# Performance work log

Measured on AMD Instinct MI355X. Metric: run time of the kernel, lower is better.

The kernel has to match this reference:

```python
import jax, jax.numpy as jnp
import numpy as np

N = 50000      # n_nodes
E = 800000     # n_edges (before self loops)
DIN = 128      # in_channels
H = 4          # heads
C = 32         # out_channels per head  (H*C == DIN -> residual is Identity)
EPS = 1e-5
NEG_SLOPE = 0.2


def layer_norm(x, g, b):
    m = jnp.mean(x, axis=-1, keepdims=True)
    v = jnp.mean((x - m) ** 2, axis=-1, keepdims=True)
    return (x - m) * jax.lax.rsqrt(v + EPS) * g + b


def setup_inputs() -> dict:
    key = jax.random.key(0)
    ks = jax.random.split(key, 14)
    s = 1.0 / np.sqrt(DIN)
    return {
        "x": jax.random.normal(ks[0], (N, DIN), dtype=jnp.float32),
        "edge_index": jax.random.randint(ks[1], (2, E), 0, N, dtype=jnp.int64),
        "ln1_g": jnp.ones((DIN,), jnp.float32),
        "ln1_b": jnp.zeros((DIN,), jnp.float32),
        "W": jax.random.normal(ks[2], (DIN, H * C), jnp.float32) * s,
        "att_src": jax.random.normal(ks[3], (H, C), jnp.float32) * (1.0 / np.sqrt(C)),
        "att_dst": jax.random.normal(ks[4], (H, C), jnp.float32) * (1.0 / np.sqrt(C)),
        "gat_b": jnp.zeros((H * C,), jnp.float32),
        "ln2_g": jnp.ones((H * C,), jnp.float32),
        "ln2_b": jnp.zeros((H * C,), jnp.float32),
        "w1": jax.random.normal(ks[5], (H * C, 2 * H * C), jnp.float32) * (1.0 / np.sqrt(H * C)),
        "b1": jnp.zeros((2 * H * C,), jnp.float32),
        "w2": jax.random.normal(ks[6], (2 * H * C, H * C), jnp.float32) * (1.0 / np.sqrt(2 * H * C)),
        "b2": jnp.zeros((H * C,), jnp.float32),
    }


def gat_conv(h, src, dst, W, att_src, att_dst, gat_b, n):
    # linear projection per head: (n, H, C)
    xh = (h @ W).reshape(n, H, C)
    # per-node attention logits: (n, H)
    a_src = jnp.einsum("nhc,hc->nh", xh, att_src)
    a_dst = jnp.einsum("nhc,hc->nh", xh, att_dst)
    # edge scores + segment softmax over destination nodes
    alpha = jax.nn.leaky_relu(a_src[src] + a_dst[dst], NEG_SLOPE)  # (e, H)
    amax = jax.ops.segment_max(alpha, dst, num_segments=n)
    alpha = jnp.exp(alpha - amax[dst])
    denom = jax.ops.segment_sum(alpha, dst, num_segments=n)
    alpha = alpha / denom[dst]
    # weighted aggregation of source features
    msg = xh[src] * alpha[:, :, None]                                # (e, H, C)
    out = jax.ops.segment_sum(msg, dst, num_segments=n)              # (n, H, C)
    return out.reshape(n, H * C) + gat_b


def reference(x, edge_index, ln1_g, ln1_b, W, att_src, att_dst, gat_b,
              ln2_g, ln2_b, w1, b1, w2, b2):
    n = x.shape[0]
    # add self loops (PyG GATConv default add_self_loops=True)
    loops = jnp.arange(n, dtype=edge_index.dtype)
    src = jnp.concatenate([edge_index[0], loops])
    dst = jnp.concatenate([edge_index[1], loops])

    h = layer_norm(x, ln1_g, ln1_b)
    h = gat_conv(h, src, dst, W, att_src, att_dst, gat_b, n)
    h = h + x  # residual is Identity since in_channels == heads*out_channels
    hn = layer_norm(h, ln2_g, ln2_b)
    ffn = jax.nn.gelu(hn @ w1 + b1, approximate=False) @ w2 + b2
    return h + ffn
```

## Files before the change

kernel.cpp:

```cpp
#include <hip/hip_runtime.h>

#define DIN 128
#define HEADS 4
#define CPH 32
#define NEG_SLOPE 0.2f
#define LN_EPS 1e-5f
#define NPB 16
#define CS 4096
#define CE 512

typedef short bf16x8 __attribute__((ext_vector_type(8)));
typedef float f32x4 __attribute__((ext_vector_type(4)));
typedef float f32x2 __attribute__((ext_vector_type(2)));

__device__ __forceinline__ float wave_allsum(float v) {
#pragma unroll
    for (int off = 32; off > 0; off >>= 1) v += __shfl_down(v, off, 64);
    return __shfl(v, 0, 64);
}

__device__ __forceinline__ unsigned short f2bf(float f) {
    unsigned int b = __float_as_uint(f);
    b += 0x7FFFu + ((b >> 16) & 1u);
    return (unsigned short)(b >> 16);
}
__device__ __forceinline__ float bf2f(unsigned short u) {
    return __uint_as_float(((unsigned int)u) << 16);
}

#define ABST 136
#define HST  264
#define SRST 132

__global__ __launch_bounds__(256) void k_hist_pack(
    const int* __restrict__ ei, unsigned int* __restrict__ cnt, int E, int Et, int HB,
    const float* __restrict__ w1, const float* __restrict__ w2, const float* __restrict__ W,
    unsigned short* __restrict__ wp1, unsigned short* __restrict__ wp2,
    unsigned short* __restrict__ wpW)
{
    int bid = blockIdx.x;
    if (bid < HB) {
        int base = bid * CS + threadIdx.x;
#pragma unroll
        for (int i = 0; i < CS / 256; ++i) {
            int e = base + i * 256;
            if (e >= Et) break;
            int d = (e < E) ? ei[E + e] : (e - E);
            atomicAdd(&cnt[d], 1u);
        }
    } else {
        int idx = (bid - HB) * 256 + threadIdx.x;
        if (idx < 32768) {
            int j = idx & 7, lane = (idx >> 3) & 63, tk = idx >> 9;
            int ks = tk & 3, tile = tk >> 2;
            int k = ks * 32 + ((lane >> 4) << 3) + j;
            int n = tile * 16 + (lane & 15);
            wp1[idx] = f2bf(w1[k * 256 + n]);
        } else if (idx < 65536) {
            int i2 = idx - 32768;
            int j = i2 & 7, lane = (i2 >> 3) & 63, tk = i2 >> 9;
            int ks = tk & 7, tile = tk >> 3;
            int k = ks * 32 + ((lane >> 4) << 3) + j;
            int n = tile * 16 + (lane & 15);
            wp2[i2] = f2bf(w2[k * 128 + n]);
        } else {
            int i3 = idx - 65536;
            int j = i3 & 7, lane = (i3 >> 3) & 63, tk = i3 >> 9;
            int ks = tk & 3, tile = tk >> 2;
            int k = ks * 32 + ((lane >> 4) << 3) + j;
            int n = tile * 16 + (lane & 15);
            wpW[i3] = f2bf(W[k * 128 + n]);
        }
    }
}

__global__ __launch_bounds__(256) void k_scan_fused(
    const unsigned int* __restrict__ cnt,
    unsigned int* __restrict__ done, unsigned int* __restrict__ flag,
    unsigned int* __restrict__ bsum, unsigned int* __restrict__ boff,
    unsigned int* __restrict__ row, unsigned int* __restrict__ pos, int N, int Et)
{
    __shared__ unsigned int ws[4];
    __shared__ unsigned int s_tot;
    __shared__ int s_last;
    __shared__ unsigned int s_base;
    int t = threadIdx.x;
    int lane = t & 63, wv = t >> 6;
    int bid = blockIdx.x;
    int nb = gridDim.x;
    int i = bid * 256 + t;

    unsigned int v = (i < N) ? cnt[i] : 0u;
    unsigned int s = v;
#pragma unroll
    for (int off = 1; off < 64; off <<= 1) {
        unsigned int a = (unsigned int)__shfl_up((int)s, off, 64);
        if (lane >= off) s += a;
    }
    if (lane == 63) ws[wv] = s;
    __syncthreads();
    if (t == 0) {
        unsigned int a0 = ws[0], a1 = ws[1], a2 = ws[2], a3 = ws[3];
        ws[0] = 0u; ws[1] = a0; ws[2] = a0 + a1; ws[3] = a0 + a1 + a2;
        s_tot = a0 + a1 + a2 + a3;
    }
    __syncthreads();
    unsigned int excl = ws[wv] + (s - v);

    if (t == 0) {
        __hip_atomic_store(&bsum[bid], s_tot, __ATOMIC_RELEASE, __HIP_MEMORY_SCOPE_AGENT);
        unsigned int old = __hip_atomic_fetch_add(done, 1u, __ATOMIC_ACQ_REL, __HIP_MEMORY_SCOPE_AGENT);
        s_last = (old == (unsigned int)(nb - 1)) ? 1 : 0;
    }
    __syncthreads();

    if (s_last) {
        unsigned int bv = (t < nb) ? __hip_atomic_load(&bsum[t], __ATOMIC_ACQUIRE, __HIP_MEMORY_SCOPE_AGENT) : 0u;
        unsigned int sc = bv;
#pragma unroll
        for (int off = 1; off < 64; off <<= 1) {
            unsigned int a = (unsigned int)__shfl_up((int)sc, off, 64);
            if (lane >= off) sc += a;
        }
        if (lane == 63) ws[wv] = sc;
        __syncthreads();
        if (t == 0) {
            unsigned int a0 = ws[0], a1 = ws[1], a2 = ws[2];
            ws[0] = 0u; ws[1] = a0; ws[2] = a0 + a1; ws[3] = a0 + a1 + a2;
        }
        __syncthreads();
        if (t < nb) boff[t] = ws[wv] + (sc - bv);
        __syncthreads();
        if (t == 0) __hip_atomic_store(flag, 1u, __ATOMIC_RELEASE, __HIP_MEMORY_SCOPE_AGENT);
    }

    if (t == 0) {
        while (__hip_atomic_load(flag, __ATOMIC_ACQUIRE, __HIP_MEMORY_SCOPE_AGENT) == 0u)
            __builtin_amdgcn_s_sleep(8);
        s_base = boff[bid];
    }
    __syncthreads();
    unsigned int base = s_base;
    if (i < N) { row[i] = base + excl; pos[i] = base + excl; }
    if (bid == 0 && t == 0) row[N] = (unsigned int)Et;
}

__global__ __launch_bounds__(256) void k_scatter_proj(
    const int* __restrict__ ei, unsigned int* __restrict__ pos,
    int* __restrict__ srcs, int E, int N, int Et, int SB,
    const float* __restrict__ x,
    const float* __restrict__ g1, const float* __restrict__ b1,
    const unsigned short* __restrict__ wpW,
    const float* __restrict__ att_src, const float* __restrict__ att_dst,
    unsigned short* __restrict__ xhb, float* __restrict__ a_src, float* __restrict__ a_dst)
{
    __shared__ __align__(16) unsigned short A_bf[NPB * ABST];
    __shared__ __align__(16) unsigned short sxh[NPB * ABST];
    int bid = blockIdx.x;
    int t = threadIdx.x;

    if (bid < SB) {
        int base = bid * CS + t;
#pragma unroll
        for (int i = 0; i < CS / 256; ++i) {
            int e = base + i * 256;
            if (e >= Et) break;
            int d = (e < E) ? ei[E + e] : (e - E);
            int s = (e < E) ? ei[e] : d;
            unsigned int p = atomicAdd(&pos[d], 1u);
            srcs[p] = s;
        }
        return;
    }

    int w = t >> 6, lane = t & 63;
    int quad = lane >> 4, l15 = lane & 15;
    int nbase = (bid - SB) * NPB;

#pragma unroll
    for (int i = 0; i < 4; ++i) {
        int nn = w * 4 + i;
        int n = nbase + nn;
        float x0 = 0.f, x1 = 0.f;
        if (n < N) { x0 = x[n * DIN + lane]; x1 = x[n * DIN + 64 + lane]; }
        float mean = wave_allsum(x0 + x1) * (1.0f / DIN);
        float d0 = x0 - mean, d1 = x1 - mean;
        float var = wave_allsum(d0 * d0 + d1 * d1) * (1.0f / DIN);
        float rstd = rsqrtf(var + LN_EPS);
        A_bf[nn * ABST + lane]      = f2bf(d0 * rstd * g1[lane]      + b1[lane]);
        A_bf[nn * ABST + 64 + lane] = f2bf(d1 * rstd * g1[64 + lane] + b1[64 + lane]);
    }
    __syncthreads();

    {
        int arow = l15 * ABST;
        bf16x8 afrag[4];
#pragma unroll
        for (int ks = 0; ks < 4; ++ks)
            afrag[ks] = *(const bf16x8*)&A_bf[arow + ks * 32 + quad * 8];
#pragma unroll
        for (int nt = 0; nt < 2; ++nt) {
            int tile = w * 2 + nt;
            f32x4 acc = {0.f, 0.f, 0.f, 0.f};
#pragma unroll
            for (int ks = 0; ks < 4; ++ks) {
                bf16x8 bfrag = *(const bf16x8*)&wpW[(((tile * 4 + ks) * 64 + lane) << 3)];
                acc = __builtin_amdgcn_mfma_f32_16x16x32_bf16(afrag[ks], bfrag, acc, 0, 0, 0);
            }
            int col = tile * 16 + l15;
#pragma unroll
            for (int reg = 0; reg < 4; ++reg)
                sxh[(quad * 4 + reg) * ABST + col] = f2bf(acc[reg]);
        }
    }
    __syncthreads();

    {
        int node = t >> 4, off = (t & 15) * 8;
        int n = nbase + node;
        if (n < N)
            *(uint4*)&xhb[(size_t)n * DIN + off] = *(const uint4*)&sxh[node * ABST + off];
    }

    {
        int node = w * 4 + (lane >> 4);
        int h = (lane >> 2) & 3, sub = lane & 3;
        float s1 = 0.f, s2 = 0.f;
#pragma unroll
        for (int i = 0; i < 8; ++i) {
            int c = h * CPH + sub * 8 + i;
            float v = bf2f(sxh[node * ABST + c]);
            s1 += v * att_src[c];
            s2 += v * att_dst[c];
        }
        s1 += __shfl_down(s1, 1, 64); s2 += __shfl_down(s2, 1, 64);
        s1 += __shfl_down(s1, 2, 64); s2 += __shfl_down(s2, 2, 64);
        int n = nbase + node;
        if (sub == 0 && n < N) {
            a_src[n * HEADS + h] = s1;
            a_dst[n * HEADS + h] = s2;
        }
    }
}

__global__ __launch_bounds__(256, 6) void k_agg_final(
    const unsigned int* __restrict__ row, const int* __restrict__ srcs,
    const float* __restrict__ a_src, const float* __restrict__ a_dst,
    const uint2* __restrict__ xhb2,
    const float* __restrict__ x,
    const float* __restrict__ gat_b,
    const float* __restrict__ g2, const float* __restrict__ b2g,
    const unsigned short* __restrict__ wp1, const float* __restrict__ bb1,
    const unsigned short* __restrict__ wp2, const float* __restrict__ bb2,
    float* __restrict__ out, int N)
{
    __shared__ __align__(16) unsigned char smem[21248];
    float*          shres  = (float*)smem;
    unsigned short* A_bf   = (unsigned short*)(smem + 8448);
    unsigned short* hid_bf = (unsigned short*)(smem + 12800);
    float*          s_p    = (float*)smem;
    int*            s_srcs = (int*)(smem + 8192);
    float*          s_adl  = (float*)(smem + 10240);
    int*            s_rowl = (int*)(smem + 10496);

    int t = threadIdx.x;
    int w = t >> 6, lane = t & 63;
    int quad = lane >> 4, l15 = lane & 15;
    int nbase = blockIdx.x * NPB;
    int half = lane >> 5;
    int li   = lane & 31;
    int h2   = li >> 3;

    f32x2 gbp, g2p, b2p;
    {
        const f32x2* gb2 = (const f32x2*)gat_b;
        const f32x2* gg2 = (const f32x2*)g2;
        const f32x2* bb2v = (const f32x2*)b2g;
        gbp = gb2[lane]; g2p = gg2[lane]; b2p = bb2v[lane];
    }

    if (t <= NPB) {
        int idx = nbase + t; if (idx > N) idx = N;
        s_rowl[t] = (int)row[idx];
    }
    if (t < 64) {
        int d = nbase + (t >> 2);
        s_adl[t] = (d < N) ? a_dst[d * HEADS + (t & 3)] : 0.f;
    }

    int nend = nbase + NPB; if (nend > N) nend = N;
    int estart = (int)row[nbase];
    int eend = (int)row[nend];

    int wr[5];
#pragma unroll
    for (int j = 0; j < 5; ++j) {
        int idx = nbase + w * 4 + j; if (idx > N) idx = N;
        wr[j] = (int)row[idx];
    }

    float o4[4][4];
    float den4[4];
#pragma unroll
    for (int i = 0; i < 4; ++i) {
        den4[i] = 0.f;
#pragma unroll
        for (int c = 0; c < 4; ++c) o4[i][c] = 0.f;
    }

    for (int cbase = estart; cbase < eend; cbase += CE) {
        int cnum = eend - cbase; if (cnum > CE) cnum = CE;
        int cend = cbase + cnum;
        __syncthreads();

        for (int e = t; e < cnum; e += 256) {
            int ge = cbase + e;
            int s = srcs[ge];
            s_srcs[e] = s;
            int node = 0;
#pragma unroll
            for (int k = 1; k <= NPB; ++k) node += (ge >= s_rowl[k]) ? 1 : 0;
            float4 as4 = *(const float4*)&a_src[s * 4];
            float4 ad4 = *(const float4*)&s_adl[node * 4];
            float4 pv;
            float a0 = as4.x + ad4.x; a0 = fmaxf(a0, NEG_SLOPE * a0); pv.x = __expf(a0);
            float a1 = as4.y + ad4.y; a1 = fmaxf(a1, NEG_SLOPE * a1); pv.y = __expf(a1);
            float a2 = as4.z + ad4.z; a2 = fmaxf(a2, NEG_SLOPE * a2); pv.z = __expf(a2);
            float a3 = as4.w + ad4.w; a3 = fmaxf(a3, NEG_SLOPE * a3); pv.w = __expf(a3);
            *(float4*)&s_p[e * 4] = pv;
        }
        __syncthreads();

#pragma unroll
        for (int i = 0; i < 4; ++i) {
            int lo = wr[i] > cbase ? wr[i] : cbase;
            int hi = wr[i + 1] < cend ? wr[i + 1] : cend;
            if (lo >= hi) continue;
            int e = lo - cbase;
            int eh = hi - cbase;
            float p0_ = o4[i][0], p1_ = o4[i][1], p2_ = o4[i][2], p3_ = o4[i][3];
            float den_ = den4[i];
            for (; e + 16 <= eh; e += 16) {
                uint2 uu[8]; float pp[8];
#pragma unroll
                for (int j = 0; j < 8; ++j) {
                    int s = s_srcs[e + 2 * j + half];
                    uu[j] = xhb2[s * 32 + li];
                }
#pragma unroll
                for (int j = 0; j < 8; ++j) pp[j] = s_p[((e + 2 * j + half) << 2) + h2];
#pragma unroll
                for (int j = 0; j < 8; ++j) {
                    den_ += pp[j];
                    p0_ += pp[j] * __uint_as_float(uu[j].x << 16);
                    p1_ += pp[j] * __uint_as_float(uu[j].x & 0xFFFF0000u);
                    p2_ += pp[j] * __uint_as_float(uu[j].y << 16);
                    p3_ += pp[j] * __uint_as_float(uu[j].y & 0xFFFF0000u);
                }
            }
            for (; e + 8 <= eh; e += 8) {
                uint2 uu[4]; float pp[4];
#pragma unroll
                for (int j = 0; j < 4; ++j) {
                    int s = s_srcs[e + 2 * j + half];
                    uu[j] = xhb2[s * 32 + li];
                }
#pragma unroll
                for (int j = 0; j < 4; ++j) pp[j] = s_p[((e + 2 * j + half) << 2) + h2];
#pragma unroll
                for (int j = 0; j < 4; ++j) {
                    den_ += pp[j];
                    p0_ += pp[j] * __uint_as_float(uu[j].x << 16);
                    p1_ += pp[j] * __uint_as_float(uu[j].x & 0xFFFF0000u);
                    p2_ += pp[j] * __uint_as_float(uu[j].y << 16);
                    p3_ += pp[j] * __uint_as_float(uu[j].y & 0xFFFF0000u);
                }
            }
            for (; e + 2 <= eh; e += 2) {
                int s = s_srcs[e + half];
                float p = s_p[((e + half) << 2) + h2];
                uint2 u = xhb2[s * 32 + li];
                den_ += p;
                p0_ += p * __uint_as_float(u.x << 16);
                p1_ += p * __uint_as_float(u.x & 0xFFFF0000u);
                p2_ += p * __uint_as_float(u.y << 16);
                p3_ += p * __uint_as_float(u.y & 0xFFFF0000u);
            }
            if (e < eh) {
                int s = s_srcs[e];
                float p = half ? 0.f : s_p[(e << 2) + h2];
                uint2 u = xhb2[s * 32 + li];
                den_ += p;
                p0_ += p * __uint_as_float(u.x << 16);
                p1_ += p * __uint_as_float(u.x & 0xFFFF0000u);
                p2_ += p * __uint_as_float(u.y << 16);
                p3_ += p * __uint_as_float(u.y & 0xFFFF0000u);
            }
            o4[i][0] = p0_; o4[i][1] = p1_; o4[i][2] = p2_; o4[i][3] = p3_;
            den4[i] = den_;
        }
    }
    __syncthreads();

#pragma unroll
    for (int i = 0; i < 4; ++i) {
        int nn = w * 4 + i;
        int d = nbase + nn;
        float c0 = o4[i][0] + __shfl_xor(o4[i][0], 32, 64);
        float c1 = o4[i][1] + __shfl_xor(o4[i][1], 32, 64);
        float c2 = o4[i][2] + __shfl_xor(o4[i][2], 32, 64);
        float c3 = o4[i][3] + __shfl_xor(o4[i][3], 32, 64);
        float dn = den4[i] + __shfl_xor(den4[i], 32, 64);
        int srcl = lane >> 1;
        float a0 = __shfl(c0, srcl, 64);
        float a1 = __shfl(c1, srcl, 64);
        float a2 = __shfl(c2, srcl, 64);
        float a3 = __shfl(c3, srcl, 64);
        float den_p = __shfl(dn, (lane >> 4) << 3, 64);
        float oo0 = (lane & 1) ? a2 : a0;
        float oo1 = (lane & 1) ? a3 : a1;

        float h0 = 0.f, h1 = 0.f;
        if (d < N) {
            float inv = 1.0f / den_p;
            f32x2 xv = ((const f32x2*)(x + (size_t)d * DIN))[lane];
            h0 = oo0 * inv + gbp.x + xv.x;
            h1 = oo1 * inv + gbp.y + xv.y;
        }
        float mean = wave_allsum(h0 + h1) * (1.0f / DIN);
        float d0 = h0 - mean, d1 = h1 - mean;
        float var = wave_allsum(d0 * d0 + d1 * d1) * (1.0f / DIN);
        float rstd = rsqrtf(var + LN_EPS);
        f32x2 hres; hres.x = h0; hres.y = h1;
        ((f32x2*)&shres[nn * SRST])[lane] = hres;
        unsigned int apk = (unsigned int)f2bf(d0 * rstd * g2p.x + b2p.x)
                         | ((unsigned int)f2bf(d1 * rstd * g2p.y + b2p.y) << 16);
        ((unsigned int*)&A_bf[nn * ABST])[lane] = apk;
    }
    __syncthreads();

    {
        int arow = l15 * ABST;
        bf16x8 afrag[4];
#pragma unroll
        for (int ks = 0; ks < 4; ++ks)
            afrag[ks] = *(const bf16x8*)&A_bf[arow + ks * 32 + quad * 8];
#pragma unroll
        for (int nt = 0; nt < 4; ++nt) {
            int tile = w * 4 + nt;
            f32x4 acc = {0.f, 0.f, 0.f, 0.f};
#pragma unroll
            for (int ks = 0; ks < 4; ++ks) {
                bf16x8 bfrag = *(const bf16x8*)&wp1[(((tile * 4 + ks) * 64 + lane) << 3)];
                acc = __builtin_amdgcn_mfma_f32_16x16x32_bf16(afrag[ks], bfrag, acc, 0, 0, 0);
            }
            int col = tile * 16 + l15;
            float bias = bb1[col];
#pragma unroll
            for (int reg = 0; reg < 4; ++reg) {
                int m_local = quad * 4 + reg;
                float a = acc[reg] + bias;
                float g = 0.5f * a * (1.0f + erff(a * 0.70710678118654752f));
                hid_bf[m_local * HST + col] = f2bf(g);
            }
        }
    }
    __syncthreads();

    {
        int arow = l15 * HST;
        bf16x8 afrag[8];
#pragma unroll
        for (int ks = 0; ks < 8; ++ks)
            afrag[ks] = *(const bf16x8*)&hid_bf[arow + ks * 32 + quad * 8];
#pragma unroll
        for (int nt = 0; nt < 2; ++nt) {
            int tile = w * 2 + nt;
            f32x4 acc = {0.f, 0.f, 0.f, 0.f};
#pragma unroll
            for (int ks = 0; ks < 8; ++ks) {
                bf16x8 bfrag = *(const bf16x8*)&wp2[(((tile * 8 + ks) * 64 + lane) << 3)];
                acc = __builtin_amdgcn_mfma_f32_16x16x32_bf16(afrag[ks], bfrag, acc, 0, 0, 0);
            }
            int j = tile * 16 + l15;
            float bias = bb2[j];
#pragma unroll
            for (int reg = 0; reg < 4; ++reg) {
                int m_local = quad * 4 + reg;
                int n = nbase + m_local;
                if (n < N)
                    out[(size_t)n * DIN + j] = shres[m_local * SRST + j] + acc[reg] + bias;
            }
        }
    }
}

extern "C" void kernel_launch(void* const* d_in, const int* in_sizes, int n_in,
                              void* d_out, int out_size, void* d_ws, size_t ws_size,
                              hipStream_t stream) {
    const float* x       = (const float*)d_in[0];
    const int*   ei      = (const int*)d_in[1];
    const float* ln1_g   = (const float*)d_in[2];
    const float* ln1_b   = (const float*)d_in[3];
    const float* W       = (const float*)d_in[4];
    const float* att_src = (const float*)d_in[5];
    const float* att_dst = (const float*)d_in[6];
    const float* gat_b   = (const float*)d_in[7];
    const float* ln2_g   = (const float*)d_in[8];
    const float* ln2_b   = (const float*)d_in[9];
    const float* w1      = (const float*)d_in[10];
    const float* b1      = (const float*)d_in[11];
    const float* w2      = (const float*)d_in[12];
    const float* b2      = (const float*)d_in[13];
    float* out = (float*)d_out;

    const int N = in_sizes[0] / DIN;
    const int E = in_sizes[1] / 2;
    const int Et = E + N;

    unsigned short* wp1 = (unsigned short*)d_ws;
    unsigned short* wp2 = wp1 + 32768;
    unsigned short* wpW = wp2 + 32768;
    unsigned short* xhb = wpW + 16384;
    float*        a_src = (float*)(xhb + (size_t)N * DIN);
    float*        a_dst = a_src + (size_t)N * HEADS;
    unsigned int* cnt  = (unsigned int*)(a_dst + (size_t)N * HEADS);
    unsigned int* done = cnt + N;
    unsigned int* flag = done + 1;
    unsigned int* row  = flag + 1;
    unsigned int* pos  = row + N + 1;
    unsigned int* bsum = pos + N;
    unsigned int* boff = bsum + 256;
    int*           srcs = (int*)(boff + 256);

    hipMemsetAsync(cnt, 0, (size_t)(N + 2) * sizeof(unsigned int), stream);

    int nblocks = (N + NPB - 1) / NPB;
    int cblocks = (Et + CS - 1) / CS;
    int nb2 = (N + 255) / 256;

    k_hist_pack<<<cblocks + 320, 256, 0, stream>>>(ei, cnt, E, Et, cblocks, w1, w2, W, wp1, wp2, wpW);

    k_scan_fused<<<nb2, 256, 0, stream>>>(cnt, done, flag, bsum, boff, row, pos, N, Et);

    k_scatter_proj<<<cblocks + nblocks, 256, 0, stream>>>(ei, pos, srcs, E, N, Et, cblocks,
                                                          x, ln1_g, ln1_b, wpW, att_src, att_dst,
                                                          xhb, a_src, a_dst);

    k_agg_final<<<nblocks, 256, 0, stream>>>(row, srcs, a_src, a_dst, (const uint2*)xhb,
                                             x, gat_b, ln2_g, ln2_b, wp1, b1, wp2, b2, out, N);
}
```

Baseline: 262.3 us.

## Partition histogram/scatter atomics by XCD and fuse scan into projection kernel

Histogram and scatter blocks are replicated eight times, and each copy only handles destinations in one eighth of the node range. The copy is chosen by bid&7, so that the atomics for a node range stay on one XCD's L2. The separate scan kernel is merged into the scatter/projection kernel, and the scatter blocks spin-wait on a scan_done counter. This costs eight times more edge-index reads and adds inter-block spin waits, which assume the scan blocks get scheduled first.

```diff
diff --git a/kernel.cpp b/kernel.cpp
--- a/kernel.cpp
+++ b/kernel.cpp
@@ -33,20 +33,23 @@
 #define SRST 132
 
 __global__ __launch_bounds__(256) void k_hist_pack(
-    const int* __restrict__ ei, unsigned int* __restrict__ cnt, int E, int Et, int HB,
+    const int* __restrict__ ei, unsigned int* __restrict__ cnt, int E, int N, int Nper, int HB,
     const float* __restrict__ w1, const float* __restrict__ w2, const float* __restrict__ W,
     unsigned short* __restrict__ wp1, unsigned short* __restrict__ wp2,
     unsigned short* __restrict__ wpW)
 {
     int bid = blockIdx.x;
     if (bid < HB) {
-        int base = bid * CS + threadIdx.x;
+        int xcd = bid & 7, chunk = bid >> 3;
+        int lo = xcd * Nper, hi = min(lo + Nper, N);
+        int Et = E + N;
+        int base = chunk * CS + threadIdx.x;
 #pragma unroll
         for (int i = 0; i < CS / 256; ++i) {
             int e = base + i * 256;
             if (e >= Et) break;
             int d = (e < E) ? ei[E + e] : (e - E);
-            atomicAdd(&cnt[d], 1u);
+            if (d >= lo && d < hi) atomicAdd(&cnt[d], 1u);
         }
     } else {
         int idx = (bid - HB) * 256 + threadIdx.x;
@@ -74,80 +77,14 @@
     }
 }
 
-__global__ __launch_bounds__(256) void k_scan_fused(
+__global__ __launch_bounds__(256) void k_build_proj(
     const unsigned int* __restrict__ cnt,
     unsigned int* __restrict__ done, unsigned int* __restrict__ flag,
+    unsigned int* __restrict__ scan_done,
     unsigned int* __restrict__ bsum, unsigned int* __restrict__ boff,
-    unsigned int* __restrict__ row, unsigned int* __restrict__ pos, int N, int Et)
-{
-    __shared__ unsigned int ws[4];
-    __shared__ unsigned int s_tot;
-    __shared__ int s_last;
-    __shared__ unsigned int s_base;
-    int t = threadIdx.x;
-    int lane = t & 63, wv = t >> 6;
-    int bid = blockIdx.x;
-    int nb = gridDim.x;
-    int i = bid * 256 + t;
-
-    unsigned int v = (i < N) ? cnt[i] : 0u;
-    unsigned int s = v;
-#pragma unroll
-    for (int off = 1; off < 64; off <<= 1) {
-        unsigned int a = (unsigned int)__shfl_up((int)s, off, 64);
-        if (lane >= off) s += a;
-    }
-    if (lane == 63) ws[wv] = s;
-    __syncthreads();
-    if (t == 0) {
-        unsigned int a0 = ws[0], a1 = ws[1], a2 = ws[2], a3 = ws[3];
-        ws[0] = 0u; ws[1] = a0; ws[2] = a0 + a1; ws[3] = a0 + a1 + a2;
-        s_tot = a0 + a1 + a2 + a3;
-    }
-    __syncthreads();
-    unsigned int excl = ws[wv] + (s - v);
-
-    if (t == 0) {
-        __hip_atomic_store(&bsum[bid], s_tot, __ATOMIC_RELEASE, __HIP_MEMORY_SCOPE_AGENT);
-        unsigned int old = __hip_atomic_fetch_add(done, 1u, __ATOMIC_ACQ_REL, __HIP_MEMORY_SCOPE_AGENT);
-        s_last = (old == (unsigned int)(nb - 1)) ? 1 : 0;
-    }
-    __syncthreads();
-
-    if (s_last) {
-        unsigned int bv = (t < nb) ? __hip_atomic_load(&bsum[t], __ATOMIC_ACQUIRE, __HIP_MEMORY_SCOPE_AGENT) : 0u;
-        unsigned int sc = bv;
-#pragma unroll
-        for (int off = 1; off < 64; off <<= 1) {
-            unsigned int a = (unsigned int)__shfl_up((int)sc, off, 64);
-            if (lane >= off) sc += a;
-        }
-        if (lane == 63) ws[wv] = sc;
-        __syncthreads();
-        if (t == 0) {
-            unsigned int a0 = ws[0], a1 = ws[1], a2 = ws[2];
-            ws[0] = 0u; ws[1] = a0; ws[2] = a0 + a1; ws[3] = a0 + a1 + a2;
-        }
-        __syncthreads();
-        if (t < nb) boff[t] = ws[wv] + (sc - bv);
-        __syncthreads();
-        if (t == 0) __hip_atomic_store(flag, 1u, __ATOMIC_RELEASE, __HIP_MEMORY_SCOPE_AGENT);
-    }
-
-    if (t == 0) {
-        while (__hip_atomic_load(flag, __ATOMIC_ACQUIRE, __HIP_MEMORY_SCOPE_AGENT) == 0u)
-            __builtin_amdgcn_s_sleep(8);
-        s_base = boff[bid];
-    }
-    __syncthreads();
-    unsigned int base = s_base;
-    if (i < N) { row[i] = base + excl; pos[i] = base + excl; }
-    if (bid == 0 && t == 0) row[N] = (unsigned int)Et;
-}
-
-__global__ __launch_bounds__(256) void k_scatter_proj(
-    const int* __restrict__ ei, unsigned int* __restrict__ pos,
-    int* __restrict__ srcs, int E, int N, int Et, int SB,
+    unsigned int* __restrict__ row, unsigned int* __restrict__ pos,
+    const int* __restrict__ ei, int* __restrict__ srcs,
+    int E, int N, int Et, int Nper, int SCB, int SB,
     const float* __restrict__ x,
     const float* __restrict__ g1, const float* __restrict__ b1,
     const unsigned short* __restrict__ wpW,
@@ -156,26 +93,106 @@
 {
     __shared__ __align__(16) unsigned short A_bf[NPB * ABST];
     __shared__ __align__(16) unsigned short sxh[NPB * ABST];
+    __shared__ unsigned int ws[4];
+    __shared__ unsigned int s_tot;
+    __shared__ int s_last;
+    __shared__ unsigned int s_base;
+
     int bid = blockIdx.x;
     int t = threadIdx.x;
 
-    if (bid < SB) {
-        int base = bid * CS + t;
+    if (bid < SCB) {
+        int lane = t & 63, wv = t >> 6;
+        int i = bid * 256 + t;
+        unsigned int v = (i < N) ? cnt[i] : 0u;
+        unsigned int s = v;
+#pragma unroll
+        for (int off = 1; off < 64; off <<= 1) {
+            unsigned int a = (unsigned int)__shfl_up((int)s, off, 64);
+            if (lane >= off) s += a;
+        }
+        if (lane == 63) ws[wv] = s;
+        __syncthreads();
+        if (t == 0) {
+            unsigned int a0 = ws[0], a1 = ws[1], a2 = ws[2], a3 = ws[3];
+            ws[0] = 0u; ws[1] = a0; ws[2] = a0 + a1; ws[3] = a0 + a1 + a2;
+            s_tot = a0 + a1 + a2 + a3;
+        }
+        __syncthreads();
+        unsigned int excl = ws[wv] + (s - v);
+
+        if (t == 0) {
+            __hip_atomic_store(&bsum[bid], s_tot, __ATOMIC_RELEASE, __HIP_MEMORY_SCOPE_AGENT);
+            unsigned int old = __hip_atomic_fetch_add(done, 1u, __ATOMIC_ACQ_REL, __HIP_MEMORY_SCOPE_AGENT);
+            s_last = (old == (unsigned int)(SCB - 1)) ? 1 : 0;
+        }
+        __syncthreads();
+
+        if (s_last) {
+            int lane2 = t & 63, wv2 = t >> 6;
+            unsigned int bv = (t < SCB) ? __hip_atomic_load(&bsum[t], __ATOMIC_ACQUIRE, __HIP_MEMORY_SCOPE_AGENT) : 0u;
+            unsigned int sc = bv;
+#pragma unroll
+            for (int off = 1; off < 64; off <<= 1) {
+                unsigned int a = (unsigned int)__shfl_up((int)sc, off, 64);
+                if (lane2 >= off) sc += a;
+            }
+            if (lane2 == 63) ws[wv2] = sc;
+            __syncthreads();
+            if (t == 0) {
+                unsigned int a0 = ws[0], a1 = ws[1], a2 = ws[2];
+                ws[0] = 0u; ws[1] = a0; ws[2] = a0 + a1; ws[3] = a0 + a1 + a2;
+            }
+            __syncthreads();
+            if (t < SCB) boff[t] = ws[wv2] + (sc - bv);
+            __syncthreads();
+            if (t == 0) __hip_atomic_store(flag, 1u, __ATOMIC_RELEASE, __HIP_MEMORY_SCOPE_AGENT);
+        }
+
+        if (t == 0) {
+            while (__hip_atomic_load(flag, __ATOMIC_ACQUIRE, __HIP_MEMORY_SCOPE_AGENT) == 0u)
+                __builtin_amdgcn_s_sleep(8);
+            s_base = boff[bid];
+        }
+        __syncthreads();
+        unsigned int base = s_base;
+        if (i < N) { row[i] = base + excl; pos[i] = base + excl; }
+        if (bid == 0 && t == 0) row[N] = (unsigned int)Et;
+        __syncthreads();
+        if (t == 0) {
+            __threadfence();
+            __hip_atomic_fetch_add(scan_done, 1u, __ATOMIC_ACQ_REL, __HIP_MEMORY_SCOPE_AGENT);
+        }
+        return;
+    }
+
+    if (bid < SCB + SB) {
+        if (t == 0) {
+            while (__hip_atomic_load(scan_done, __ATOMIC_ACQUIRE, __HIP_MEMORY_SCOPE_AGENT) < (unsigned int)SCB)
+                __builtin_amdgcn_s_sleep(16);
+        }
+        __syncthreads();
+        int bid2 = bid - SCB;
+        int xcd = bid2 & 7, chunk = bid2 >> 3;
+        int lo = xcd * Nper, hi = min(lo + Nper, N);
+        int base = chunk * CS + t;
 #pragma unroll
         for (int i = 0; i < CS / 256; ++i) {
             int e = base + i * 256;
             if (e >= Et) break;
             int d = (e < E) ? ei[E + e] : (e - E);
-            int s = (e < E) ? ei[e] : d;
-            unsigned int p = atomicAdd(&pos[d], 1u);
-            srcs[p] = s;
+            if (d >= lo && d < hi) {
+                int s = (e < E) ? ei[e] : d;
+                unsigned int p = atomicAdd(&pos[d], 1u);
+                srcs[p] = s;
+            }
         }
         return;
     }
 
     int w = t >> 6, lane = t & 63;
     int quad = lane >> 4, l15 = lane & 15;
-    int nbase = (bid - SB) * NPB;
+    int nbase = (bid - SCB - SB) * NPB;
 
 #pragma unroll
     for (int i = 0; i < 4; ++i) {
@@ -517,6 +534,7 @@
     const int N = in_sizes[0] / DIN;
     const int E = in_sizes[1] / 2;
     const int Et = E + N;
+    const int Nper = (N + 7) / 8;
 
     unsigned short* wp1 = (unsigned short*)d_ws;
     unsigned short* wp2 = wp1 + 32768;
@@ -527,25 +545,26 @@
     unsigned int* cnt  = (unsigned int*)(a_dst + (size_t)N * HEADS);
     unsigned int* done = cnt + N;
     unsigned int* flag = done + 1;
-    unsigned int* row  = flag + 1;
+    unsigned int* scan_done = flag + 1;
+    unsigned int* row  = scan_done + 1;
     unsigned int* pos  = row + N + 1;
     unsigned int* bsum = pos + N;
     unsigned int* boff = bsum + 256;
     int*           srcs = (int*)(boff + 256);
 
-    hipMemsetAsync(cnt, 0, (size_t)(N + 2) * sizeof(unsigned int), stream);
+    hipMemsetAsync(cnt, 0, (size_t)(N + 3) * sizeof(unsigned int), stream);
 
     int nblocks = (N + NPB - 1) / NPB;
     int cblocks = (Et + CS - 1) / CS;
-    int nb2 = (N + 255) / 256;
-
-    k_hist_pack<<<cblocks + 320, 256, 0, stream>>>(ei, cnt, E, Et, cblocks, w1, w2, W, wp1, wp2, wpW);
-
-    k_scan_fused<<<nb2, 256, 0, stream>>>(cnt, done, flag, bsum, boff, row, pos, N, Et);
-
-    k_scatter_proj<<<cblocks + nblocks, 256, 0, stream>>>(ei, pos, srcs, E, N, Et, cblocks,
-                                                          x, ln1_g, ln1_b, wpW, att_src, att_dst,
-                                                          xhb, a_src, a_dst);
+    int HB = cblocks * 8;
+    int SCB = (N + 255) / 256;
+
+    k_hist_pack<<<HB + 320, 256, 0, stream>>>(ei, cnt, E, N, Nper, HB, w1, w2, W, wp1, wp2, wpW);
+
+    k_build_proj<<<SCB + HB + nblocks, 256, 0, stream>>>(
+        cnt, done, flag, scan_done, bsum, boff, row, pos,
+        ei, srcs, E, N, Et, Nper, SCB, HB,
+        x, ln1_g, ln1_b, wpW, att_src, att_dst, xhb, a_src, a_dst);
 
     k_agg_final<<<nblocks, 256, 0, stream>>>(row, srcs, a_src, a_dst, (const uint2*)xhb,
                                              x, gat_b, ln2_g, ln2_b, wp1, b1, wp2, b2, out, N);
```

New measurement: 426.2 us. 62.5% more time.

## Pre-bucket edges by destination range before CSR scatter for locality

Applied to the files above, without the earlier changes.

The histogram kernel now also partitions edges into 8 buckets by destination-node range, writing (src,dst) pairs into per-bucket arrays through block-local counters. The scatter phase then walks each bucket with a fixed grid of 26 blocks per bucket, so the atomics on pos and the writes to srcs hit a narrow node range and should get better L2 locality. In exchange the edge list is read twice in the first kernel and an extra bucket buffer is written and read back. Bucket capacity is fixed at Et/8+16384, which can overflow if destinations are skewed.

```diff
diff --git a/kernel.cpp b/kernel.cpp
--- a/kernel.cpp
+++ b/kernel.cpp
@@ -8,6 +8,7 @@
 #define NPB 16
 #define CS 4096
 #define CE 512
+#define KB 26
 
 typedef short bf16x8 __attribute__((ext_vector_type(8)));
 typedef float f32x4 __attribute__((ext_vector_type(4)));
@@ -32,24 +33,51 @@
 #define HST  264
 #define SRST 132
 
-__global__ __launch_bounds__(256) void k_hist_pack(
-    const int* __restrict__ ei, unsigned int* __restrict__ cnt, int E, int Et, int HB,
+__global__ __launch_bounds__(256) void k_bucket_pack(
+    const int* __restrict__ ei, unsigned int* __restrict__ cnt,
+    unsigned int* __restrict__ bktoff, uint2* __restrict__ bkt,
+    int E, int N, int Et, int Nper, int capb, int HB,
     const float* __restrict__ w1, const float* __restrict__ w2, const float* __restrict__ W,
     unsigned short* __restrict__ wp1, unsigned short* __restrict__ wp2,
     unsigned short* __restrict__ wpW)
 {
     int bid = blockIdx.x;
+    int t = threadIdx.x;
     if (bid < HB) {
-        int base = bid * CS + threadIdx.x;
+        __shared__ unsigned int lcnt[8];
+        __shared__ unsigned int lbase[8];
+        if (t < 8) lcnt[t] = 0u;
+        __syncthreads();
+        int base = bid * CS;
 #pragma unroll
         for (int i = 0; i < CS / 256; ++i) {
-            int e = base + i * 256;
-            if (e >= Et) break;
-            int d = (e < E) ? ei[E + e] : (e - E);
-            atomicAdd(&cnt[d], 1u);
+            int e = base + i * 256 + t;
+            if (e < Et) {
+                int d = (e < E) ? ei[E + e] : (e - E);
+                int b = min((unsigned)d / (unsigned)Nper, 7u);
+                atomicAdd(&lcnt[b], 1u);
+                atomicAdd(&cnt[d], 1u);
+            }
+        }
+        __syncthreads();
+        if (t < 8) {
+            lbase[t] = atomicAdd(&bktoff[t], lcnt[t]);
+            lcnt[t] = 0u;
+        }
+        __syncthreads();
+#pragma unroll
+        for (int i = 0; i < CS / 256; ++i) {
+            int e = base + i * 256 + t;
+            if (e < Et) {
+                int d = (e < E) ? ei[E + e] : (e - E);
+                int s = (e < E) ? ei[e] : d;
+                int b = min((unsigned)d / (unsigned)Nper, 7u);
+                unsigned int idx = lbase[b] + atomicAdd(&lcnt[b], 1u);
+                bkt[(size_t)b * capb + idx] = make_uint2((unsigned int)s, (unsigned int)d);
+            }
         }
     } else {
-        int idx = (bid - HB) * 256 + threadIdx.x;
+        int idx = (bid - HB) * 256 + t;
         if (idx < 32768) {
             int j = idx & 7, lane = (idx >> 3) & 63, tk = idx >> 9;
             int ks = tk & 3, tile = tk >> 2;
@@ -146,8 +174,8 @@
 }
 
 __global__ __launch_bounds__(256) void k_scatter_proj(
-    const int* __restrict__ ei, unsigned int* __restrict__ pos,
-    int* __restrict__ srcs, int E, int N, int Et, int SB,
+    const uint2* __restrict__ bkt, const unsigned int* __restrict__ bktoff, int capb,
+    unsigned int* __restrict__ pos, int* __restrict__ srcs, int N, int SB,
     const float* __restrict__ x,
     const float* __restrict__ g1, const float* __restrict__ b1,
     const unsigned short* __restrict__ wpW,
@@ -160,15 +188,13 @@
     int t = threadIdx.x;
 
     if (bid < SB) {
-        int base = bid * CS + t;
-#pragma unroll
-        for (int i = 0; i < CS / 256; ++i) {
-            int e = base + i * 256;
-            if (e >= Et) break;
-            int d = (e < E) ? ei[E + e] : (e - E);
-            int s = (e < E) ? ei[e] : d;
-            unsigned int p = atomicAdd(&pos[d], 1u);
-            srcs[p] = s;
+        int b = bid & 7, c = bid >> 3;
+        unsigned int len = bktoff[b];
+        const uint2* mybkt = bkt + (size_t)b * capb;
+        for (unsigned int i = (unsigned int)c * 256u + t; i < len; i += (unsigned int)KB * 256u) {
+            uint2 sd = mybkt[i];
+            unsigned int p = atomicAdd(&pos[sd.y], 1u);
+            srcs[p] = (int)sd.x;
         }
         return;
     }
@@ -517,6 +543,8 @@
     const int N = in_sizes[0] / DIN;
     const int E = in_sizes[1] / 2;
     const int Et = E + N;
+    const int Nper = (N + 7) / 8;
+    const int capb = Et / 8 + 16384;
 
     unsigned short* wp1 = (unsigned short*)d_ws;
     unsigned short* wp2 = wp1 + 32768;
@@ -527,25 +555,30 @@
     unsigned int* cnt  = (unsigned int*)(a_dst + (size_t)N * HEADS);
     unsigned int* done = cnt + N;
     unsigned int* flag = done + 1;
-    unsigned int* row  = flag + 1;
+    unsigned int* bktoff = flag + 1;
+    unsigned int* row  = bktoff + 8;
     unsigned int* pos  = row + N + 1;
     unsigned int* bsum = pos + N;
     unsigned int* boff = bsum + 256;
     int*           srcs = (int*)(boff + 256);
-
-    hipMemsetAsync(cnt, 0, (size_t)(N + 2) * sizeof(unsigned int), stream);
+    uint2*         bkt  = (uint2*)(((size_t)(srcs + Et) + 15) & ~(size_t)15);
+
+    hipMemsetAsync(cnt, 0, (size_t)(N + 10) * sizeof(unsigned int), stream);
 
     int nblocks = (N + NPB - 1) / NPB;
     int cblocks = (Et + CS - 1) / CS;
-    int nb2 = (N + 255) / 256;
-
-    k_hist_pack<<<cblocks + 320, 256, 0, stream>>>(ei, cnt, E, Et, cblocks, w1, w2, W, wp1, wp2, wpW);
-
-    k_scan_fused<<<nb2, 256, 0, stream>>>(cnt, done, flag, bsum, boff, row, pos, N, Et);
-
-    k_scatter_proj<<<cblocks + nblocks, 256, 0, stream>>>(ei, pos, srcs, E, N, Et, cblocks,
-                                                          x, ln1_g, ln1_b, wpW, att_src, att_dst,
-                                                          xhb, a_src, a_dst);
+    int SCB = (N + 255) / 256;
+    int SB = 8 * KB;
+
+    k_bucket_pack<<<cblocks + 320, 256, 0, stream>>>(ei, cnt, bktoff, bkt,
+                                                     E, N, Et, Nper, capb, cblocks,
+                                                     w1, w2, W, wp1, wp2, wpW);
+
+    k_scan_fused<<<SCB, 256, 0, stream>>>(cnt, done, flag, bsum, boff, row, pos, N, Et);
+
+    k_scatter_proj<<<SB + nblocks, 256, 0, stream>>>(bkt, bktoff, capb, pos, srcs, N, SB,
+                                                     x, ln1_g, ln1_b, wpW, att_src, att_dst,
+                                                     xhb, a_src, a_dst);
 
     k_agg_final<<<nblocks, 256, 0, stream>>>(row, srcs, a_src, a_dst, (const uint2*)xhb,
                                              x, gat_b, ln2_g, ln2_b, wp1, b1, wp2, b2, out, N);
```

Result: slower. 268.7 us (+2.5%).
